# Kernel optimization log

Measured on AMD Instinct MI355X. Metric: run time of the kernel, lower is better.

The kernel has to match this reference:

```python
import jax, jax.numpy as jnp
import numpy as np
import math

D_MODEL = 512

def setup_inputs() -> dict:
    key = jax.random.key(0)
    k1, k2, k3 = jax.random.split(key, 3)
    X = jax.random.normal(k1, (4, 8192, D_MODEL), dtype=jnp.float32)
    # nn.Linear(d, d, bias=False) weights, applied as x @ W.T
    s = 1.0 / math.sqrt(D_MODEL)
    W_v = jax.random.uniform(k2, (D_MODEL, D_MODEL), dtype=jnp.float32, minval=-s, maxval=s)
    W_theta = jax.random.uniform(k3, (D_MODEL, D_MODEL), dtype=jnp.float32, minval=-s, maxval=s)
    return {"X": X, "W_v": W_v, "W_theta": W_theta}

def reference(X, W_v, W_theta):
    # X: [B, n, d]
    n = X.shape[1]
    d = X.shape[2]
    XW_v = X @ W_v.T            # [B, n, d]
    theta_X = X @ W_theta.T     # [B, n, d]
    # first term: (1/n) * ones(n,n) @ XW_v == column mean broadcast over rows
    first_term = jnp.mean(XW_v, axis=1, keepdims=True)  # [B, 1, d], broadcasts
    # second term: (1/(n*sqrt(d))) * (X @ theta_X^T) @ XW_v
    # associativity-reduced: theta_X^T @ XW_v is [B, d, d]
    kv = jnp.einsum('bnd,bne->bde', theta_X, XW_v)       # [B, d, d]
    second_term = (X @ kv) / (n * math.sqrt(d))          # [B, n, d]
    return first_term + second_term
```

## Files before the change

### kernel.cpp

```cpp
#include <hip/hip_runtime.h>
#include <stdint.h>


typedef __bf16 bf16x8 __attribute__((ext_vector_type(8)));
typedef float f32x4 __attribute__((ext_vector_type(4)));
typedef unsigned short u16x4 __attribute__((ext_vector_type(4)));
typedef unsigned short u16x8 __attribute__((ext_vector_type(8)));

#define BK 32

#define BAR asm volatile("s_barrier" ::: "memory")

template <int N>
__device__ __forceinline__ void vmw() {
  static_assert(N == 0 || N == 1 || N == 2 || N == 4 || N == 8, "vmw");
  if constexpr (N == 0) asm volatile("s_waitcnt vmcnt(0)" ::: "memory");
  else if constexpr (N == 1) asm volatile("s_waitcnt vmcnt(1)" ::: "memory");
  else if constexpr (N == 2) asm volatile("s_waitcnt vmcnt(2)" ::: "memory");
  else if constexpr (N == 4) asm volatile("s_waitcnt vmcnt(4)" ::: "memory");
  else if constexpr (N == 8) asm volatile("s_waitcnt vmcnt(8)" ::: "memory");
}

__device__ __forceinline__ unsigned short f2bf(float f) {
  union { float f; unsigned int u; } c; c.f = f;
  unsigned int u = c.u;
  return (unsigned short)((u + 0x7FFFu + ((u >> 16) & 1u)) >> 16);
}
__device__ __forceinline__ float bf2f(unsigned short h) {
  union { unsigned int u; float f; } c; c.u = ((unsigned int)h) << 16;
  return c.f;
}

__device__ __forceinline__ void gld16(const void* g, void* l) {
  using gptr_t = const __attribute__((address_space(1))) void*;
  using lptr_t = __attribute__((address_space(3))) void*;
  __builtin_amdgcn_global_load_lds((gptr_t)(uintptr_t)g,
                                   (lptr_t)(uint32_t)(uintptr_t)l, 16, 0, 0);
}

template <int TB, bool SAME>
__device__ __forceinline__ void gemm_tile(const unsigned short* __restrict__ A, int lda,
                                          const unsigned short* __restrict__ B, int ldb,
                                          int m0, int n0, f32x4 (&acc)[TB / 32][TB / 32]) {
  static_assert(TB == 64 || TB == 128, "TB");
  constexpr int FR = TB / 32;
  constexpr int LJ = (TB * 4) / 256;
  constexpr int LPS = SAME ? LJ : 2 * LJ;
  constexpr int NK = 512 / BK;
  __shared__ unsigned short sA[3][TB * BK];
  __shared__ unsigned short sB[3][TB * BK];
  const int tid = threadIdx.x;
  const int lane = tid & 63;
  const int w = tid >> 6;
  const int wm = w >> 1, wn = w & 1;
  const int quad = lane >> 4, l16 = lane & 15;
  const int sq = (quad ^ ((l16 >> 1) & 3)) * 8;

#pragma unroll
  for (int mi = 0; mi < FR; mi++)
#pragma unroll
    for (int ni = 0; ni < FR; ni++) acc[mi][ni] = f32x4{0.f, 0.f, 0.f, 0.f};

  auto stage = [&](int bb, int kt) {
    const int kk = kt * BK;
#pragma unroll
    for (int j = 0; j < LJ; j++) {
      const int slot = w * (LJ * 64) + j * 64 + lane;
      const int row = slot >> 2;
      const int col = ((slot & 3) ^ ((slot >> 3) & 3)) * 8;
      const int basegr = w * (LJ * 64) + j * 64;
      gld16(A + (size_t)(m0 + row) * lda + kk + col, (char*)sA[bb] + (size_t)basegr * 16);
      if constexpr (!SAME)
        gld16(B + (size_t)(n0 + row) * ldb + kk + col, (char*)sB[bb] + (size_t)basegr * 16);
    }
  };

  auto compute = [&](int bb) {
    const unsigned short* as = sA[bb];
    const unsigned short* bs = SAME ? sA[bb] : sB[bb];
    bf16x8 af[FR], bfr[FR];
#pragma unroll
    for (int mi = 0; mi < FR; mi++)
      af[mi] = *(const bf16x8*)&as[(wm * (TB / 2) + mi * 16 + l16) * BK + sq];
#pragma unroll
    for (int ni = 0; ni < FR; ni++)
      bfr[ni] = *(const bf16x8*)&bs[(wn * (TB / 2) + ni * 16 + l16) * BK + sq];
#pragma unroll
    for (int mi = 0; mi < FR; mi++)
#pragma unroll
      for (int ni = 0; ni < FR; ni++)
        acc[mi][ni] = __builtin_amdgcn_mfma_f32_16x16x32_bf16(af[mi], bfr[ni],
                                                              acc[mi][ni], 0, 0, 0);
  };

  stage(0, 0);
  stage(1, 1);
  stage(2, 2);
#pragma unroll
  for (int kt = 0; kt < NK; ++kt) {
    if (kt < NK - 2) { vmw<2 * LPS>(); }
    else if (kt == NK - 2) { vmw<LPS>(); }
    else { vmw<0>(); }
    BAR;
    compute(kt % 3);
    BAR;
    if (kt < NK - 3) stage(kt % 3, kt + 3);
  }
}

__global__ __launch_bounds__(256) void prep_kernel(const float* __restrict__ X,
                                                   unsigned short* __restrict__ Xb,
                                                   unsigned short* __restrict__ Xt,
                                                   float* __restrict__ mean_x) {
  __shared__ unsigned short sT[2][64 * 64];
  const int t = threadIdx.x;
  const int n0 = blockIdx.x * 128, d0 = blockIdx.y * 64;
  const int b = n0 >> 13, nb = n0 & 8191;
  const int r0 = (t >> 4) * 4, c0 = (t & 15) * 4;
  f32x4 v[2][4];
#pragma unroll
  for (int s = 0; s < 2; s++)
#pragma unroll
    for (int i = 0; i < 4; i++)
      v[s][i] = *(const f32x4*)(X + (size_t)(n0 + s * 64 + r0 + i) * 512 + d0 + c0);
  __builtin_amdgcn_sched_barrier(0);
  u16x4 o[2][4];
#pragma unroll
  for (int s = 0; s < 2; s++)
#pragma unroll
    for (int i = 0; i < 4; i++)
#pragma unroll
      for (int j = 0; j < 4; j++) o[s][i][j] = f2bf(v[s][i][j]);
#pragma unroll
  for (int s = 0; s < 2; s++)
#pragma unroll
    for (int j = 0; j < 4; j++) {
      u16x4 wv;
#pragma unroll
      for (int i = 0; i < 4; i++) wv[i] = o[s][i][j];
      const int c = c0 + j;
      const int rsw = r0 ^ (c & 0x38);
      *(u16x4*)&sT[s][c * 64 + rsw] = wv;
    }
  __syncthreads();
#pragma unroll
  for (int s = 0; s < 2; s++)
#pragma unroll
    for (int i = 0; i < 4; i++)
      *(u16x4*)(Xb + (size_t)(n0 + s * 64 + r0 + i) * 512 + d0 + c0) = o[s][i];
  const int cr = t >> 3, p = t & 7;
  float csum[2] = {0.f, 0.f};
#pragma unroll
  for (int s = 0; s < 2; s++)
#pragma unroll
    for (int h = 0; h < 2; h++) {
      const int c = cr + h * 32;
      const int phys = (p * 8) ^ (c & 0x38);
      u16x8 val = *(const u16x8*)&sT[s][c * 64 + phys];
      *(u16x8*)(Xt + (size_t)(b * 512 + d0 + c) * 8192 + nb + s * 64 + p * 8) = val;
      float ss = 0.f;
#pragma unroll
      for (int j = 0; j < 8; j++) ss += bf2f(val[j]);
      csum[h] += ss;
    }
#pragma unroll
  for (int h = 0; h < 2; h++) {
    float sv = csum[h];
    sv += __shfl_xor(sv, 1);
    sv += __shfl_xor(sv, 2);
    sv += __shfl_xor(sv, 4);
    if (p == 0) atomicAdd(&mean_x[b * 512 + d0 + cr + h * 32], sv);
  }
}

__global__ __launch_bounds__(256) void prep_w_kernel(const float* __restrict__ Wv,
                                                     const float* __restrict__ Wth,
                                                     unsigned short* __restrict__ Wvb,
                                                     unsigned short* __restrict__ Wtb,
                                                     float* __restrict__ mean_x) {
  const int blk = blockIdx.x;
  const int t = threadIdx.x;
  if (blk == 0) {
#pragma unroll
    for (int i = 0; i < 8; i++) mean_x[t + i * 256] = 0.f;
  }
  const float* src = (blk < 128) ? Wv : Wth;
  unsigned short* dst = (blk < 128) ? Wvb : Wtb;
  const int i = (blk & 127) * 256 + t;
  const f32x4* pp = (const f32x4*)(src + (size_t)i * 8);
  f32x4 v0 = pp[0], v1 = pp[1];
  u16x8 o;
  o[0] = f2bf(v0[0]); o[1] = f2bf(v0[1]); o[2] = f2bf(v0[2]); o[3] = f2bf(v0[3]);
  o[4] = f2bf(v1[0]); o[5] = f2bf(v1[1]); o[6] = f2bf(v1[2]); o[7] = f2bf(v1[3]);
  *(u16x8*)(dst + (size_t)i * 8) = o;
}

static __device__ const int TI[10] = {0, 0, 0, 0, 1, 1, 1, 2, 2, 3};
static __device__ const int TJ[10] = {0, 1, 2, 3, 1, 2, 3, 2, 3, 3};

__global__ __launch_bounds__(256) void g_gemm_kernel(const unsigned short* __restrict__ Xt,
                                                     float* __restrict__ G_part) {
  const int t = blockIdx.x;
  const int z = blockIdx.y;
  const int b = z >> 4, s = z & 15;
  const int m0 = TI[t] * 128, n0 = TJ[t] * 128;
  const unsigned short* A = Xt + (size_t)b * 512 * 8192 + (size_t)s * 512;
  f32x4 acc[4][4];
  if (m0 == n0)
    gemm_tile<128, true>(A, 8192, A, 8192, m0, n0, acc);
  else
    gemm_tile<128, false>(A, 8192, A, 8192, m0, n0, acc);
  float* Cp = G_part + ((size_t)z * 10 + t) * 16384;
  const int tid = threadIdx.x, lane = tid & 63, w = tid >> 6;
  const int wm = w >> 1, wn = w & 1, quad = lane >> 4, l16 = lane & 15;
#pragma unroll
  for (int mi = 0; mi < 4; mi++)
#pragma unroll
    for (int ni = 0; ni < 4; ni++) {
      const int ml = wm * 64 + mi * 16 + quad * 4;
      const int nl = wn * 64 + ni * 16 + l16;
      *(f32x4*)(Cp + (size_t)nl * 128 + ml) = acc[mi][ni];
    }
}

__global__ __launch_bounds__(256) void g_fin_kernel(const float* __restrict__ G_part,
                                                    unsigned short* __restrict__ Gb,
                                                    const float* __restrict__ mean_x,
                                                    const float* __restrict__ Wv,
                                                    float* __restrict__ meanV) {
  const int blk = blockIdx.x;
  if (blk >= 320) {
    const int idx = (blk - 320) * 256 + threadIdx.x;
    const int b = idx >> 9, e = idx & 511;
    const float* mx = mean_x + b * 512;
    const float* wr = Wv + (size_t)e * 512;
    float s = 0.f;
    for (int d = 0; d < 512; d += 4) {
      f32x4 a = *(const f32x4*)(mx + d);
      f32x4 w4 = *(const f32x4*)(wr + d);
      s += a[0] * w4[0] + a[1] * w4[1] + a[2] * w4[2] + a[3] * w4[3];
    }
    meanV[idx] = s * (1.f / 8192.f);
    return;
  }
  const int b = blk / 80, rem = blk % 80;
  const int t = rem >> 3, cc = rem & 7;
  const int i = TI[t], j = TJ[t];
  const int m0 = i * 128, n0 = j * 128;
  const int tid = threadIdx.x;
  const int np = cc * 16 + (tid >> 4);
  const int mp = (tid & 15) * 8;
  f32x4 s0 = f32x4{0.f, 0.f, 0.f, 0.f}, s1 = f32x4{0.f, 0.f, 0.f, 0.f};
#pragma unroll
  for (int s = 0; s < 16; s++) {
    const float* p = G_part + (((size_t)(b * 16 + s)) * 10 + t) * 16384 + (size_t)np * 128 + mp;
    s0 += *(const f32x4*)p;
    s1 += *(const f32x4*)(p + 4);
  }
  const float scale = (float)(1.0 / (8192.0 * 22.627416997969522));
  unsigned short h[8];
#pragma unroll
  for (int r = 0; r < 4; r++) { h[r] = f2bf(s0[r] * scale); h[r + 4] = f2bf(s1[r] * scale); }
  unsigned short* Gbb = Gb + (size_t)b * 262144;
#pragma unroll
  for (int r = 0; r < 8; r++)
    Gbb[(size_t)(m0 + mp + r) * 512 + (n0 + np)] = h[r];
  if (i != j) {
    u16x8 o;
#pragma unroll
    for (int r = 0; r < 8; r++) o[r] = h[r];
    *(u16x8*)(Gbb + (size_t)(n0 + np) * 512 + (m0 + mp)) = o;
  }
}

__global__ __launch_bounds__(256) void gemm_rm_kernel(const unsigned short* __restrict__ A,
                                                      const unsigned short* __restrict__ B,
                                                      unsigned short* __restrict__ C,
                                                      size_t Abs, size_t Bbs) {
  const int b = blockIdx.z;
  const int m0 = blockIdx.x * 64, n0 = blockIdx.y * 64;
  f32x4 acc[2][2];
  gemm_tile<64, false>(A + (size_t)b * Abs, 512, B + (size_t)b * Bbs, 512, m0, n0, acc);
  unsigned short* Cb = C + (size_t)b * 262144;
  const int tid = threadIdx.x, lane = tid & 63, w = tid >> 6;
  const int wm = w >> 1, wn = w & 1, quad = lane >> 4, l16 = lane & 15;
#pragma unroll
  for (int mi = 0; mi < 2; mi++)
#pragma unroll
    for (int ni = 0; ni < 2; ni++) {
      const int m = m0 + wm * 32 + mi * 16 + quad * 4;
      const int n = n0 + wn * 32 + ni * 16 + l16;
#pragma unroll
      for (int r = 0; r < 4; r++)
        Cb[(size_t)(m + r) * 512 + n] = f2bf(acc[mi][ni][r]);
    }
}

__global__ __launch_bounds__(256) void gemm_out_kernel(
    const unsigned short* __restrict__ Xb, const unsigned short* __restrict__ kvt,
    const float* __restrict__ meanV, float* __restrict__ out) {
  const int m0 = blockIdx.x * 128, n0 = blockIdx.y * 128;
  const int b = blockIdx.x >> 6;
  const unsigned short* Bm = kvt + (size_t)b * 262144;
  f32x4 acc[4][4];
  gemm_tile<128, false>(Xb, 512, Bm, 512, m0, n0, acc);
  const int tid = threadIdx.x, lane = tid & 63, w = tid >> 6;
  const int wm = w >> 1, wn = w & 1, quad = lane >> 4, l16 = lane & 15;
#pragma unroll
  for (int ni = 0; ni < 4; ni++) {
    const int e = n0 + wn * 64 + ni * 16 + l16;
    const float mu = meanV[b * 512 + e];
#pragma unroll
    for (int mi = 0; mi < 4; mi++) {
      const int m = m0 + wm * 64 + mi * 16 + quad * 4;
#pragma unroll
      for (int r = 0; r < 4; r++)
        out[(size_t)(m + r) * 512 + e] = acc[mi][ni][r] + mu;
    }
  }
}

extern "C" void kernel_launch(void* const* d_in, const int* in_sizes, int n_in,
                              void* d_out, int out_size, void* d_ws, size_t ws_size,
                              hipStream_t stream) {
  const float* X = (const float*)d_in[0];
  const float* Wv = (const float*)d_in[1];
  const float* Wth = (const float*)d_in[2];
  float* out = (float*)d_out;
  char* ws = (char*)d_ws;

  unsigned short* Xb = (unsigned short*)(ws);
  unsigned short* Xt = (unsigned short*)(ws + 33554432ull);
  float* G_part = (float*)(ws + 67108864ull);
  unsigned short* Gb = (unsigned short*)(ws + 109051904ull);
  unsigned short* Ht = (unsigned short*)(ws + 111149056ull);
  unsigned short* kvt = (unsigned short*)(ws + 113246208ull);
  unsigned short* Wvb = (unsigned short*)(ws + 115343360ull);
  unsigned short* Wtb = (unsigned short*)(ws + 115867648ull);
  float* mean_x = (float*)(ws + 116391936ull);
  float* meanV = (float*)(ws + 116400128ull);

  prep_w_kernel<<<256, 256, 0, stream>>>(Wv, Wth, Wvb, Wtb, mean_x);
  prep_kernel<<<dim3(256, 8), 256, 0, stream>>>(X, Xb, Xt, mean_x);

  g_gemm_kernel<<<dim3(10, 64), 256, 0, stream>>>(Xt, G_part);
  g_fin_kernel<<<328, 256, 0, stream>>>(G_part, Gb, mean_x, Wv, meanV);

  gemm_rm_kernel<<<dim3(8, 8, 4), 256, 0, stream>>>(Wvb, Gb, Ht, 0, 262144);
  gemm_rm_kernel<<<dim3(8, 8, 4), 256, 0, stream>>>(Ht, Wtb, kvt, 262144, 0);

  gemm_out_kernel<<<dim3(256, 4), 256, 0, stream>>>(Xb, kvt, meanV, out);
}
```

Measured before the change: 235.1 us.

## Restructure prep transpose per-wave, swizzle GEMM block order, raise MFMA priority

The prep kernel is rewritten so each wave independently transposes a 64x32 tile through its own LDS slice, which removes the block-wide __syncthreads and changes the swizzle pattern. The g_gemm grid is transposed and gemm_out uses a 1D grid with a grouped tile order, so blocks running at the same time share operand tiles in cache. s_setprio is raised around the MFMA loop in the shared gemm tile. Together these target the prep kernel's synchronization cost and the cache reuse of the GEMMs, at the cost of more atomics per block and a scheduling change that could help or hurt.

```diff
diff --git a/kernel.cpp b/kernel.cpp
--- a/kernel.cpp
+++ b/kernel.cpp
@@ -85,12 +85,14 @@
 #pragma unroll
     for (int ni = 0; ni < FR; ni++)
       bfr[ni] = *(const bf16x8*)&bs[(wn * (TB / 2) + ni * 16 + l16) * BK + sq];
+    __builtin_amdgcn_s_setprio(1);
 #pragma unroll
     for (int mi = 0; mi < FR; mi++)
 #pragma unroll
       for (int ni = 0; ni < FR; ni++)
         acc[mi][ni] = __builtin_amdgcn_mfma_f32_16x16x32_bf16(af[mi], bfr[ni],
                                                               acc[mi][ni], 0, 0, 0);
+    __builtin_amdgcn_s_setprio(0);
   };
 
   stage(0, 0);
@@ -112,64 +114,64 @@
                                                    unsigned short* __restrict__ Xb,
                                                    unsigned short* __restrict__ Xt,
                                                    float* __restrict__ mean_x) {
-  __shared__ unsigned short sT[2][64 * 64];
+  __shared__ unsigned short sw[4][64 * 32];
   const int t = threadIdx.x;
-  const int n0 = blockIdx.x * 128, d0 = blockIdx.y * 64;
-  const int b = n0 >> 13, nb = n0 & 8191;
-  const int r0 = (t >> 4) * 4, c0 = (t & 15) * 4;
-  f32x4 v[2][4];
-#pragma unroll
-  for (int s = 0; s < 2; s++)
-#pragma unroll
-    for (int i = 0; i < 4; i++)
-      v[s][i] = *(const f32x4*)(X + (size_t)(n0 + s * 64 + r0 + i) * 512 + d0 + c0);
+  const int w = t >> 6, l = t & 63;
+  const int g = blockIdx.x * 4 + w;
+  const int d0 = (g & 15) * 32;
+  const int n64 = (g >> 4) * 64;
+  const int b = n64 >> 13, nb = n64 & 8191;
+  const int a = l >> 3, q = l & 7;
+  const int c0 = q * 4;
+  unsigned short* myw = sw[w];
+
+  f32x4 v[8];
+#pragma unroll
+  for (int i = 0; i < 8; i++)
+    v[i] = *(const f32x4*)(X + (size_t)(n64 + a + 8 * i) * 512 + d0 + c0);
   __builtin_amdgcn_sched_barrier(0);
-  u16x4 o[2][4];
-#pragma unroll
-  for (int s = 0; s < 2; s++)
-#pragma unroll
-    for (int i = 0; i < 4; i++)
-#pragma unroll
-      for (int j = 0; j < 4; j++) o[s][i][j] = f2bf(v[s][i][j]);
-#pragma unroll
-  for (int s = 0; s < 2; s++)
-#pragma unroll
-    for (int j = 0; j < 4; j++) {
-      u16x4 wv;
-#pragma unroll
-      for (int i = 0; i < 4; i++) wv[i] = o[s][i][j];
-      const int c = c0 + j;
-      const int rsw = r0 ^ (c & 0x38);
-      *(u16x4*)&sT[s][c * 64 + rsw] = wv;
-    }
-  __syncthreads();
-#pragma unroll
-  for (int s = 0; s < 2; s++)
-#pragma unroll
-    for (int i = 0; i < 4; i++)
-      *(u16x4*)(Xb + (size_t)(n0 + s * 64 + r0 + i) * 512 + d0 + c0) = o[s][i];
-  const int cr = t >> 3, p = t & 7;
-  float csum[2] = {0.f, 0.f};
-#pragma unroll
-  for (int s = 0; s < 2; s++)
-#pragma unroll
-    for (int h = 0; h < 2; h++) {
-      const int c = cr + h * 32;
-      const int phys = (p * 8) ^ (c & 0x38);
-      u16x8 val = *(const u16x8*)&sT[s][c * 64 + phys];
-      *(u16x8*)(Xt + (size_t)(b * 512 + d0 + c) * 8192 + nb + s * 64 + p * 8) = val;
-      float ss = 0.f;
-#pragma unroll
-      for (int j = 0; j < 8; j++) ss += bf2f(val[j]);
-      csum[h] += ss;
-    }
-#pragma unroll
-  for (int h = 0; h < 2; h++) {
-    float sv = csum[h];
+
+  u16x4 o[8];
+#pragma unroll
+  for (int i = 0; i < 8; i++)
+#pragma unroll
+    for (int j = 0; j < 4; j++) o[i][j] = f2bf(v[i][j]);
+
+#pragma unroll
+  for (int j = 0; j < 4; j++) {
+    u16x8 wv;
+#pragma unroll
+    for (int i = 0; i < 8; i++) wv[i] = o[i][j];
+    const int c = c0 + j;
+    const int pos = a ^ ((c >> 2) & 7);
+    *(u16x8*)&myw[c * 64 + pos * 8] = wv;
+  }
+
+#pragma unroll
+  for (int i = 0; i < 8; i++)
+    *(u16x4*)(Xb + (size_t)(n64 + a + 8 * i) * 512 + d0 + c0) = o[i];
+
+  asm volatile("s_waitcnt lgkmcnt(0)" ::: "memory");
+
+  float cs[4];
+#pragma unroll
+  for (int h = 0; h < 4; h++) {
+    const int cp = a + 8 * h;
+    const int pos = q ^ ((cp >> 2) & 7);
+    u16x8 val = *(const u16x8*)&myw[cp * 64 + pos * 8];
+    *(u16x8*)(Xt + (size_t)(b * 512 + d0 + cp) * 8192 + nb + q * 8) = val;
+    float ss = 0.f;
+#pragma unroll
+    for (int jj = 0; jj < 8; jj++) ss += bf2f(val[jj]);
+    cs[h] = ss;
+  }
+#pragma unroll
+  for (int h = 0; h < 4; h++) {
+    float sv = cs[h];
     sv += __shfl_xor(sv, 1);
     sv += __shfl_xor(sv, 2);
     sv += __shfl_xor(sv, 4);
-    if (p == 0) atomicAdd(&mean_x[b * 512 + d0 + cr + h * 32], sv);
+    if (q == 0) atomicAdd(&mean_x[b * 512 + d0 + a + 8 * h], sv);
   }
 }
 
@@ -200,8 +202,8 @@
 
 __global__ __launch_bounds__(256) void g_gemm_kernel(const unsigned short* __restrict__ Xt,
                                                      float* __restrict__ G_part) {
-  const int t = blockIdx.x;
-  const int z = blockIdx.y;
+  const int t = blockIdx.y;
+  const int z = blockIdx.x;
   const int b = z >> 4, s = z & 15;
   const int m0 = TI[t] * 128, n0 = TJ[t] * 128;
   const unsigned short* A = Xt + (size_t)b * 512 * 8192 + (size_t)s * 512;
@@ -299,8 +301,11 @@
 __global__ __launch_bounds__(256) void gemm_out_kernel(
     const unsigned short* __restrict__ Xb, const unsigned short* __restrict__ kvt,
     const float* __restrict__ meanV, float* __restrict__ out) {
-  const int m0 = blockIdx.x * 128, n0 = blockIdx.y * 128;
-  const int b = blockIdx.x >> 6;
+  const int D = blockIdx.x;
+  const int gm = (D & 7) + ((D >> 5) << 3);
+  const int nt = (D >> 3) & 3;
+  const int m0 = gm * 128, n0 = nt * 128;
+  const int b = gm >> 6;
   const unsigned short* Bm = kvt + (size_t)b * 262144;
   f32x4 acc[4][4];
   gemm_tile<128, false>(Xb, 512, Bm, 512, m0, n0, acc);
@@ -341,13 +346,13 @@
   float* meanV = (float*)(ws + 116400128ull);
 
   prep_w_kernel<<<256, 256, 0, stream>>>(Wv, Wth, Wvb, Wtb, mean_x);
-  prep_kernel<<<dim3(256, 8), 256, 0, stream>>>(X, Xb, Xt, mean_x);
-
-  g_gemm_kernel<<<dim3(10, 64), 256, 0, stream>>>(Xt, G_part);
+  prep_kernel<<<2048, 256, 0, stream>>>(X, Xb, Xt, mean_x);
+
+  g_gemm_kernel<<<dim3(64, 10), 256, 0, stream>>>(Xt, G_part);
   g_fin_kernel<<<328, 256, 0, stream>>>(G_part, Gb, mean_x, Wv, meanV);
 
   gemm_rm_kernel<<<dim3(8, 8, 4), 256, 0, stream>>>(Wvb, Gb, Ht, 0, 262144);
   gemm_rm_kernel<<<dim3(8, 8, 4), 256, 0, stream>>>(Ht, Wtb, kvt, 262144, 0);
 
-  gemm_out_kernel<<<dim3(256, 4), 256, 0, stream>>>(Xb, kvt, meanV, out);
-}
+  gemm_out_kernel<<<1024, 256, 0, stream>>>(Xb, kvt, meanV, out);
+}
```

Result: faster. 216.1 us (-8.1%).
